# Kernel optimization log

Hardware: AMD Instinct MI355X
Metric: run time of the kernel (lower is better)

## Reference

```python
import jax, jax.numpy as jnp
import numpy as np

# Constraint of the (buggy) original module: batch N == num_heads H == embed_size E, head_dim = 1,
# and value_len == key_len == query_len == L.
E = 64   # embed_size == num_heads == batch
H = 64
N = 64
L = 256
LN_EPS = 1e-5


def setup_inputs() -> dict:
    key = jax.random.key(0)
    ks = jax.random.split(key, 4)
    return {
        "values": jax.random.normal(ks[0], (N, L, E), dtype=jnp.float32),
        "keys": jax.random.normal(ks[1], (N, L, E), dtype=jnp.float32),
        "query": jax.random.normal(ks[2], (N, L, E), dtype=jnp.float32),
        # fc_out params (torch nn.Linear: y = x @ W.T + b)
        "W_out": jax.random.normal(ks[3], (E, E), dtype=jnp.float32) / np.float32(np.sqrt(E)),
        "b_out": jnp.zeros((E,), dtype=jnp.float32),
        # LayerNorm params
        "ln_w": jnp.ones((E,), dtype=jnp.float32),
        "ln_b": jnp.zeros((E,), dtype=jnp.float32),
    }


def reference(values, keys, query, W_out, b_out, ln_w, ln_b):
    Nb, Lq, Emb = query.shape
    Hh = H
    hd = Emb // Hh  # == 1

    def split_heads(x):
        # [N, L, E] -> [N, L, H, hd] -> permute(2,0,1,3) -> [H, N, L, hd]
        return x.reshape(Nb, -1, Hh, hd).transpose(2, 0, 1, 3)

    v = split_heads(values)   # [H, N, Lv, hd]
    k = split_heads(keys)     # [H, N, Lk, hd]
    q = split_heads(query)    # [H, N, Lq, hd]

    # torch.einsum('qnhd,knhd->qnk') on [H,N,L,hd] tensors: contract over (seq, head_dim)
    energy = jnp.einsum('anld,bnld->anb', q, k)            # [H, N, H]
    attn = jax.nn.softmax(energy / jnp.sqrt(jnp.float32(hd)), axis=-1)

    # torch.einsum('qnk,nkhd->qnhd') with values [H,N,Lv,hd]; requires N == H
    out = jnp.einsum('qnk,nkld->qnld', attn, v)            # [H, N, Lv, hd]

    # permute(1,2,0,3) -> [N, Lv, H, hd] -> view(N, Lq, E)
    out = out.transpose(1, 2, 0, 3).reshape(Nb, Lq, Emb)
    out = out @ W_out.T + b_out                            # fc_out, [N, Lq, E]

    # residual against the PERMUTED query [H,N,L,1] broadcasts to [H, N, Lq, E]
    x = out + q

    mu = jnp.mean(x, axis=-1, keepdims=True)
    var = jnp.var(x, axis=-1, keepdims=True)
    return (x - mu) / jnp.sqrt(var + LN_EPS) * ln_w + ln_b
```

## Files before the change

### kernel.cpp

```cpp
#include <hip/hip_runtime.h>
#include <stdint.h>

#define L_SEQ 256
#define E_DIM 64
#define N_B   64
#define LN_EPS 1e-5f

typedef float f4 __attribute__((ext_vector_type(4)));
typedef float f2 __attribute__((ext_vector_type(2)));

__global__ __launch_bounds__(512) void attn_p_kernel(
    const float* __restrict__ gq,
    const float* __restrict__ gk,
    const float* __restrict__ gw,
    float*       __restrict__ wsP)
{
    __shared__ float lds[32768];
    float* Qs    = lds;
    float* Ks    = lds + 16384;
    float* attnS = lds;
    float* WtS   = lds + 4096;

    const int t = threadIdx.x;
    const int n = blockIdx.x;
    const float* qb = gq + (size_t)n * (L_SEQ * E_DIM);
    const float* kb = gk + (size_t)n * (L_SEQ * E_DIM);

    #pragma unroll
    for (int i = 0; i < 8; ++i) {
        reinterpret_cast<f4*>(Qs)[t + 512 * i] =
            reinterpret_cast<const f4*>(qb)[t + 512 * i];
        reinterpret_cast<f4*>(Ks)[t + 512 * i] =
            reinterpret_cast<const f4*>(kb)[t + 512 * i];
    }
    __syncthreads();

    const int tx = t & 15, ty = t >> 4;
    const int b0 = tx * 4, a0 = ty * 2;

    float acc[2][4] = {};
    #pragma unroll 8
    for (int l = 0; l < L_SEQ; ++l) {
        f2 qa = *reinterpret_cast<const f2*>(&Qs[l * E_DIM + a0]);
        f4 kv = *reinterpret_cast<const f4*>(&Ks[l * E_DIM + b0]);
        #pragma unroll
        for (int ia = 0; ia < 2; ++ia)
            #pragma unroll
            for (int ib = 0; ib < 4; ++ib)
                acc[ia][ib] = fmaf(qa[ia], kv[ib], acc[ia][ib]);
    }

    #pragma unroll
    for (int ia = 0; ia < 2; ++ia) {
        float m = fmaxf(fmaxf(acc[ia][0], acc[ia][1]),
                        fmaxf(acc[ia][2], acc[ia][3]));
        #pragma unroll
        for (int s = 1; s <= 8; s <<= 1) m = fmaxf(m, __shfl_xor(m, s));
        float e0v = __expf(acc[ia][0] - m);
        float e1v = __expf(acc[ia][1] - m);
        float e2v = __expf(acc[ia][2] - m);
        float e3v = __expf(acc[ia][3] - m);
        float ssum = (e0v + e1v) + (e2v + e3v);
        #pragma unroll
        for (int s = 1; s <= 8; s <<= 1) ssum += __shfl_xor(ssum, s);
        float inv = 1.0f / ssum;
        acc[ia][0] = e0v * inv; acc[ia][1] = e1v * inv;
        acc[ia][2] = e2v * inv; acc[ia][3] = e3v * inv;
    }

    __syncthreads();

    #pragma unroll
    for (int ia = 0; ia < 2; ++ia) {
        f4 v4 = {acc[ia][0], acc[ia][1], acc[ia][2], acc[ia][3]};
        *reinterpret_cast<f4*>(&attnS[(a0 + ia) * 64 + b0]) = v4;
    }

    #pragma unroll
    for (int i = 0; i < 8; ++i) {
        int idx = t + 512 * i;
        WtS[(idx & 63) * 68 + (idx >> 6)] = gw[idx];
    }
    __syncthreads();

    const int k0 = ty * 2, e0 = tx * 4;
    float pacc[2][4] = {};
    #pragma unroll 8
    for (int q = 0; q < 64; ++q) {
        f2 av = *reinterpret_cast<const f2*>(&attnS[q * 64 + k0]);
        f4 wv = *reinterpret_cast<const f4*>(&WtS[q * 68 + e0]);
        #pragma unroll
        for (int ik = 0; ik < 2; ++ik)
            #pragma unroll
            for (int ie = 0; ie < 4; ++ie)
                pacc[ik][ie] = fmaf(av[ik], wv[ie], pacc[ik][ie]);
    }
    float* pb = wsP + (size_t)n * 4096 + e0;
    #pragma unroll
    for (int ik = 0; ik < 2; ++ik) {
        f4 v4 = {pacc[ik][0], pacc[ik][1], pacc[ik][2], pacc[ik][3]};
        *reinterpret_cast<f4*>(pb + (size_t)(k0 + ik) * 64) = v4;
    }
}

__global__ __launch_bounds__(256) void fc_ln_bcast_kernel(
    const float* __restrict__ gv,
    const float* __restrict__ gbo,
    const float* __restrict__ glnw,
    const float* __restrict__ glnb,
    const float* __restrict__ wsP,
    float*       __restrict__ gout)
{
    __shared__ float PS[64 * 64];
    __shared__ float VnS[64 * 16];

    const int t  = threadIdx.x;
    const int b  = blockIdx.x;
    const int n  = b >> 4;
    const int l0 = (b & 15) * 16;

    const f4* psrc = reinterpret_cast<const f4*>(wsP + (size_t)n * 4096);
    #pragma unroll
    for (int i = 0; i < 4; ++i)
        reinterpret_cast<f4*>(PS)[t + 256 * i] = psrc[t + 256 * i];

    #pragma unroll
    for (int i = 0; i < 4; ++i) {
        int idx = t + 256 * i;
        int lp = idx & 15, k = idx >> 4;
        VnS[k * 16 + lp] =
            gv[(size_t)k * (L_SEQ * E_DIM) + (size_t)(l0 + lp) * E_DIM + n];
    }
    __syncthreads();

    const int tx = t & 15, ty = t >> 4;
    const int e0 = tx * 4;

    float fc0 = 0.f, fc1 = 0.f, fc2 = 0.f, fc3 = 0.f;
    #pragma unroll 8
    for (int k = 0; k < 64; ++k) {
        float v = VnS[k * 16 + ty];
        f4 p4 = *reinterpret_cast<const f4*>(&PS[k * 64 + e0]);
        fc0 = fmaf(v, p4[0], fc0);
        fc1 = fmaf(v, p4[1], fc1);
        fc2 = fmaf(v, p4[2], fc2);
        fc3 = fmaf(v, p4[3], fc3);
    }

    f4 be = *reinterpret_cast<const f4*>(&gbo[e0]);
    f4 lw = *reinterpret_cast<const f4*>(&glnw[e0]);
    f4 lb = *reinterpret_cast<const f4*>(&glnb[e0]);

    float v0 = fc0 + be[0];
    float v1 = fc1 + be[1];
    float v2 = fc2 + be[2];
    float v3 = fc3 + be[3];

    float s1 = (v0 + v1) + (v2 + v3);
    float s2 = (v0 * v0 + v1 * v1) + (v2 * v2 + v3 * v3);
    #pragma unroll
    for (int s = 1; s <= 8; s <<= 1) {
        s1 += __shfl_xor(s1, s);
        s2 += __shfl_xor(s2, s);
    }
    float mu  = s1 * (1.0f / 64.0f);
    float var = s2 * (1.0f / 64.0f) - mu * mu;
    float rs  = rsqrtf(var + LN_EPS);
    f4 o;
    o[0] = (v0 - mu) * rs * lw[0] + lb[0];
    o[1] = (v1 - mu) * rs * lw[1] + lb[1];
    o[2] = (v2 - mu) * rs * lw[2] + lb[2];
    o[3] = (v3 - mu) * rs * lw[3] + lb[3];

    float* op = gout + (size_t)n * (L_SEQ * E_DIM)
                     + (size_t)(l0 + ty) * E_DIM + e0;
    const size_t hstride = (size_t)N_B * L_SEQ * E_DIM;
    #pragma unroll 8
    for (int h = 0; h < 64; ++h) {
        __builtin_nontemporal_store(o, reinterpret_cast<f4*>(op));
        op += hstride;
    }
}

extern "C" void kernel_launch(void* const* d_in, const int* in_sizes, int n_in,
                              void* d_out, int out_size, void* d_ws, size_t ws_size,
                              hipStream_t stream)
{
    const float* gv  = (const float*)d_in[0];
    const float* gk  = (const float*)d_in[1];
    const float* gq  = (const float*)d_in[2];
    const float* gw  = (const float*)d_in[3];
    const float* gbo = (const float*)d_in[4];
    const float* glw = (const float*)d_in[5];
    const float* glb = (const float*)d_in[6];
    float* wsP = (float*)d_ws;
    float* out = (float*)d_out;

    hipLaunchKernelGGL(attn_p_kernel, dim3(64), dim3(512), 0, stream,
                       gq, gk, gw, wsP);
    hipLaunchKernelGGL(fc_ln_bcast_kernel, dim3(1024), dim3(256), 0, stream,
                       gv, gbo, glw, glb, wsP, out);
}
```

Before: 311.4 us.

## Split broadcast store into separate copy kernel and enlarge attention per-thread tile

The fused LN kernel used to write its normalized tile 64 times with a strided per-head store loop. Now it writes the tile once to a workspace, and a new bcast kernel streams contiguous 32K-float4 chunks into each head slice with coalesced nontemporal stores over 2048 blocks. The attention kernel also moves to 256 threads with a 4x4 register tile instead of 2x4. This adds a third launch and an extra 4 MB workspace round-trip in exchange for more regular, more parallel output writes.

Result: faster. 304.9 us (-2.1%).

```diff
diff --git a/kernel.cpp b/kernel.cpp
--- a/kernel.cpp
+++ b/kernel.cpp
@@ -7,9 +7,8 @@
 #define LN_EPS 1e-5f
 
 typedef float f4 __attribute__((ext_vector_type(4)));
-typedef float f2 __attribute__((ext_vector_type(2)));
-
-__global__ __launch_bounds__(512) void attn_p_kernel(
+
+__global__ __launch_bounds__(256) void attn_p_kernel(
     const float* __restrict__ gq,
     const float* __restrict__ gk,
     const float* __restrict__ gw,
@@ -27,31 +26,31 @@
     const float* kb = gk + (size_t)n * (L_SEQ * E_DIM);
 
     #pragma unroll
-    for (int i = 0; i < 8; ++i) {
-        reinterpret_cast<f4*>(Qs)[t + 512 * i] =
-            reinterpret_cast<const f4*>(qb)[t + 512 * i];
-        reinterpret_cast<f4*>(Ks)[t + 512 * i] =
-            reinterpret_cast<const f4*>(kb)[t + 512 * i];
+    for (int i = 0; i < 16; ++i) {
+        reinterpret_cast<f4*>(Qs)[t + 256 * i] =
+            reinterpret_cast<const f4*>(qb)[t + 256 * i];
+        reinterpret_cast<f4*>(Ks)[t + 256 * i] =
+            reinterpret_cast<const f4*>(kb)[t + 256 * i];
     }
     __syncthreads();
 
     const int tx = t & 15, ty = t >> 4;
-    const int b0 = tx * 4, a0 = ty * 2;
-
-    float acc[2][4] = {};
+    const int b0 = tx * 4, a0 = ty * 4;
+
+    float acc[4][4] = {};
     #pragma unroll 8
     for (int l = 0; l < L_SEQ; ++l) {
-        f2 qa = *reinterpret_cast<const f2*>(&Qs[l * E_DIM + a0]);
+        f4 qa = *reinterpret_cast<const f4*>(&Qs[l * E_DIM + a0]);
         f4 kv = *reinterpret_cast<const f4*>(&Ks[l * E_DIM + b0]);
         #pragma unroll
-        for (int ia = 0; ia < 2; ++ia)
+        for (int ia = 0; ia < 4; ++ia)
             #pragma unroll
             for (int ib = 0; ib < 4; ++ib)
                 acc[ia][ib] = fmaf(qa[ia], kv[ib], acc[ia][ib]);
     }
 
     #pragma unroll
-    for (int ia = 0; ia < 2; ++ia) {
+    for (int ia = 0; ia < 4; ++ia) {
         float m = fmaxf(fmaxf(acc[ia][0], acc[ia][1]),
                         fmaxf(acc[ia][2], acc[ia][3]));
         #pragma unroll
@@ -71,45 +70,45 @@
     __syncthreads();
 
     #pragma unroll
-    for (int ia = 0; ia < 2; ++ia) {
+    for (int ia = 0; ia < 4; ++ia) {
         f4 v4 = {acc[ia][0], acc[ia][1], acc[ia][2], acc[ia][3]};
         *reinterpret_cast<f4*>(&attnS[(a0 + ia) * 64 + b0]) = v4;
     }
 
     #pragma unroll
-    for (int i = 0; i < 8; ++i) {
-        int idx = t + 512 * i;
+    for (int i = 0; i < 16; ++i) {
+        int idx = t + 256 * i;
         WtS[(idx & 63) * 68 + (idx >> 6)] = gw[idx];
     }
     __syncthreads();
 
-    const int k0 = ty * 2, e0 = tx * 4;
-    float pacc[2][4] = {};
+    const int k0 = ty * 4, e0 = tx * 4;
+    float pacc[4][4] = {};
     #pragma unroll 8
     for (int q = 0; q < 64; ++q) {
-        f2 av = *reinterpret_cast<const f2*>(&attnS[q * 64 + k0]);
+        f4 av = *reinterpret_cast<const f4*>(&attnS[q * 64 + k0]);
         f4 wv = *reinterpret_cast<const f4*>(&WtS[q * 68 + e0]);
         #pragma unroll
-        for (int ik = 0; ik < 2; ++ik)
+        for (int ik = 0; ik < 4; ++ik)
             #pragma unroll
             for (int ie = 0; ie < 4; ++ie)
                 pacc[ik][ie] = fmaf(av[ik], wv[ie], pacc[ik][ie]);
     }
     float* pb = wsP + (size_t)n * 4096 + e0;
     #pragma unroll
-    for (int ik = 0; ik < 2; ++ik) {
+    for (int ik = 0; ik < 4; ++ik) {
         f4 v4 = {pacc[ik][0], pacc[ik][1], pacc[ik][2], pacc[ik][3]};
         *reinterpret_cast<f4*>(pb + (size_t)(k0 + ik) * 64) = v4;
     }
 }
 
-__global__ __launch_bounds__(256) void fc_ln_bcast_kernel(
+__global__ __launch_bounds__(256) void fc_ln_kernel(
     const float* __restrict__ gv,
     const float* __restrict__ gbo,
     const float* __restrict__ glnw,
     const float* __restrict__ glnb,
     const float* __restrict__ wsP,
-    float*       __restrict__ gout)
+    float*       __restrict__ ws2)
 {
     __shared__ float PS[64 * 64];
     __shared__ float VnS[64 * 16];
@@ -172,13 +171,27 @@
     o[2] = (v2 - mu) * rs * lw[2] + lb[2];
     o[3] = (v3 - mu) * rs * lw[3] + lb[3];
 
-    float* op = gout + (size_t)n * (L_SEQ * E_DIM)
-                     + (size_t)(l0 + ty) * E_DIM + e0;
-    const size_t hstride = (size_t)N_B * L_SEQ * E_DIM;
-    #pragma unroll 8
-    for (int h = 0; h < 64; ++h) {
-        __builtin_nontemporal_store(o, reinterpret_cast<f4*>(op));
-        op += hstride;
+    *reinterpret_cast<f4*>(
+        ws2 + (size_t)n * 16384 + (size_t)(l0 + ty) * 64 + e0) = o;
+}
+
+__global__ __launch_bounds__(256) void bcast_kernel(
+    const float* __restrict__ ws2,
+    float*       __restrict__ gout)
+{
+    const int t = threadIdx.x;
+    const int b = blockIdx.x;
+    const int h = b >> 5;
+    const int c = b & 31;
+
+    const f4* src = reinterpret_cast<const f4*>(ws2) + (size_t)c * 8192;
+    f4*       dst = reinterpret_cast<f4*>(gout)
+                  + (size_t)h * 262144 + (size_t)c * 8192;
+
+    #pragma unroll 8
+    for (int i = 0; i < 32; ++i) {
+        int idx = t + 256 * i;
+        __builtin_nontemporal_store(src[idx], dst + idx);
     }
 }
 
@@ -194,10 +207,13 @@
     const float* glw = (const float*)d_in[5];
     const float* glb = (const float*)d_in[6];
     float* wsP = (float*)d_ws;
+    float* ws2 = wsP + 262144;
     float* out = (float*)d_out;
 
-    hipLaunchKernelGGL(attn_p_kernel, dim3(64), dim3(512), 0, stream,
+    hipLaunchKernelGGL(attn_p_kernel, dim3(64), dim3(256), 0, stream,
                        gq, gk, gw, wsP);
-    hipLaunchKernelGGL(fc_ln_bcast_kernel, dim3(1024), dim3(256), 0, stream,
-                       gv, gbo, glw, glb, wsP, out);
-}
+    hipLaunchKernelGGL(fc_ln_kernel, dim3(1024), dim3(256), 0, stream,
+                       gv, gbo, glw, glb, wsP, ws2);
+    hipLaunchKernelGGL(bcast_kernel, dim3(2048), dim3(256), 0, stream,
+                       ws2, out);
+}
```
